# Kernel tuning notes

Measured on AMD Instinct MI355X. Metric: run time of the kernel, lower is better.

## Reference

```python
import jax, jax.numpy as jnp
import numpy as np

B, D, H = 131072, 8, 128


def setup_inputs() -> dict:
    key = jax.random.key(0)
    ks = jax.random.split(key, 8)
    s1 = 1.0 / np.sqrt(D + 1)
    s2 = 1.0 / np.sqrt(H)
    return {
        "z": jax.random.normal(ks[0], (B, D), dtype=jnp.float32),
        "logp_z": jnp.zeros((B, 1), dtype=jnp.float32),
        "t": jax.random.uniform(ks[1], (1,), dtype=jnp.float32),
        "W1": jax.random.normal(ks[2], (D + 1, H), dtype=jnp.float32) * s1,
        "b1": jnp.zeros((H,), dtype=jnp.float32),
        "W2": jax.random.normal(ks[3], (H, H), dtype=jnp.float32) * s2,
        "b2": jnp.zeros((H,), dtype=jnp.float32),
        "W3": jax.random.normal(ks[4], (H, D), dtype=jnp.float32) * s2,
        "b3": jnp.zeros((D,), dtype=jnp.float32),
    }


def _net_single(z_i, t_scalar, W1, b1, W2, b2, W3, b3):
    # z_i: [D] -> dz/dt: [D]; FFJORD-style MLP on concat([z, t])
    x = jnp.concatenate([z_i, t_scalar[None]])  # [D+1]
    h = jnp.tanh(x @ W1 + b1)
    h = jnp.tanh(h @ W2 + b2)
    return h @ W3 + b3


def reference(z, logp_z, t, W1, b1, W2, b2, W3, b3):
    t_scalar = t.reshape(())

    def f_i(z_i):
        return _net_single(z_i, t_scalar, W1, b1, W2, b2, W3, b3)

    # dz/dt for every sample (batched forward)
    dz_dt = jax.vmap(f_i)(z)  # [B, D]
    # Exact Jacobian trace: fused forward-mode batched Jacobian (replaces the
    # original's D sequential autograd.grad reverse-mode calls)
    jac = jax.vmap(jax.jacfwd(f_i))(z)  # [B, D, D]
    trace = jnp.einsum("bii->b", jac)  # [B]
    dlogp_z_dt = -trace[:, None]  # [B, 1]
    return (dz_dt, dlogp_z_dt)
```

## Files before the change

kernel.cpp:

```cpp
#include <hip/hip_runtime.h>
#include <hip/hip_bf16.h>

#define BATCH 131072
#define PITCH 136

typedef __bf16 bf16x8 __attribute__((ext_vector_type(8)));
typedef float floatx4 __attribute__((ext_vector_type(4)));

__device__ __forceinline__ float fast_tanh(float x) {
    float e = __expf(2.0f * x);
    return 1.0f - 2.0f * __builtin_amdgcn_rcpf(e + 1.0f);
}


__global__ void prep_kernel(const float* __restrict__ W1,
                            const float* __restrict__ W2,
                            const float* __restrict__ W3,
                            __bf16* __restrict__ ws) {
    int idx = blockIdx.x * 256 + threadIdx.x;
    if (idx < 16384) {
        int j = idx & 7, q = (idx >> 3) & 3, n = (idx >> 5) & 127, kb = idx >> 12;
        int k = kb * 32 + q * 8 + j;
        ws[idx] = (__bf16)W2[k * 128 + n];
        float c = 0.0f;
        #pragma unroll
        for (int d = 0; d < 8; ++d) c += W3[k * 8 + d] * W1[d * 128 + n];
        ws[16384 + idx] = (__bf16)(W2[n * 128 + k] * c);
    } else if (idx < 20480) {
        int t = idx - 16384;
        int j = t & 7, q = (t >> 3) & 3, n = t >> 5;
        int k = q * 8 + j;
        ws[32768 + t] = (k < 9) ? (__bf16)W1[k * 128 + n] : (__bf16)0.0f;
    } else if (idx < 22528) {
        int t = idx - 20480;
        int j = t & 7, q = (t >> 3) & 3, n = (t >> 5) & 15, kb = t >> 9;
        int k = kb * 32 + q * 8 + j;
        ws[36864 + t] = (n < 8) ? (__bf16)W3[k * 8 + n] : (__bf16)0.0f;
    }
}

__global__ __launch_bounds__(256, 2) void cnf_main(
        const float* __restrict__ z, const float* __restrict__ t_ptr,
        const float* __restrict__ b1g, const float* __restrict__ b2g,
        const float* __restrict__ b3g, const __bf16* __restrict__ ws,
        float* __restrict__ out) {
    __shared__ __bf16 sW2s[16384];
    __shared__ __bf16 sW1s[4096];
    __shared__ float sb1[128];
    __shared__ float sb2[128];
    __shared__ __bf16 tile[4][16 * PITCH];

    const int tid = threadIdx.x;
    {
        uint4* dst = (uint4*)sW2s;
        const uint4* src = (const uint4*)ws;
        for (int i = tid; i < 2048; i += 256) dst[i] = src[i];
        uint4* dst1 = (uint4*)sW1s;
        const uint4* src1 = (const uint4*)(ws + 32768);
        for (int i = tid; i < 512; i += 256) dst1[i] = src1[i];
        if (tid < 128) { sb1[tid] = b1g[tid]; sb2[tid] = b2g[tid]; }
    }
    __syncthreads();

    const int lane = tid & 63;
    const int w = tid >> 6;
    const int p = lane & 15;
    const int q = lane >> 4;
    __bf16* T = tile[w];
    const float tval = t_ptr[0];
    const float b3v = (p < 8) ? b3g[p] : 0.0f;
    const bf16x8* W2sv = (const bf16x8*)sW2s;
    const bf16x8* W1sv = (const bf16x8*)sW1s;
    const bf16x8* GTv  = (const bf16x8*)(ws + 16384);
    const bf16x8* W3v  = (const bf16x8*)(ws + 36864);

    for (int it = 0; it < 4; ++it) {
        const int s0 = blockIdx.x * 256 + it * 64 + w * 16;

        bf16x8 ax;
        #pragma unroll
        for (int j = 0; j < 8; ++j) ax[j] = (__bf16)0.0f;
        if (q == 0) {
            const float4 z0 = ((const float4*)(z + (size_t)(s0 + p) * 8))[0];
            const float4 z1 = ((const float4*)(z + (size_t)(s0 + p) * 8))[1];
            ax[0] = (__bf16)z0.x; ax[1] = (__bf16)z0.y;
            ax[2] = (__bf16)z0.z; ax[3] = (__bf16)z0.w;
            ax[4] = (__bf16)z1.x; ax[5] = (__bf16)z1.y;
            ax[6] = (__bf16)z1.z; ax[7] = (__bf16)z1.w;
        } else if (q == 1) {
            ax[0] = (__bf16)tval;
        }

        float a1c[32];
        #pragma unroll
        for (int nt = 0; nt < 8; ++nt) {
            const int n = nt * 16 + p;
            floatx4 acc = {0.f, 0.f, 0.f, 0.f};
            acc = __builtin_amdgcn_mfma_f32_16x16x32_bf16(ax, W1sv[n * 4 + q], acc, 0, 0, 0);
            const float bn = sb1[n];
            #pragma unroll
            for (int r = 0; r < 4; ++r) {
                const float h1 = fast_tanh(acc[r] + bn);
                a1c[nt * 4 + r] = __builtin_fmaf(-h1, h1, 1.0f);
                T[(q * 4 + r) * PITCH + n] = (__bf16)h1;
            }
        }
        bf16x8 ah[4];
        #pragma unroll
        for (int kb = 0; kb < 4; ++kb)
            ah[kb] = *(const bf16x8*)&T[p * PITCH + kb * 32 + q * 8];

        float h2c[32];
        #pragma unroll
        for (int nt = 0; nt < 8; ++nt) {
            const int n = nt * 16 + p;
            floatx4 acc = {0.f, 0.f, 0.f, 0.f};
            #pragma unroll
            for (int kb = 0; kb < 4; ++kb)
                acc = __builtin_amdgcn_mfma_f32_16x16x32_bf16(
                        ah[kb], W2sv[(kb * 128 + n) * 4 + q], acc, 0, 0, 0);
            const float bn = sb2[n];
            #pragma unroll
            for (int r = 0; r < 4; ++r) {
                const float h2 = fast_tanh(acc[r] + bn);
                h2c[nt * 4 + r] = h2;
                const float a2 = __builtin_fmaf(-h2, h2, 1.0f);
                T[(q * 4 + r) * PITCH + n] = (__bf16)a2;
            }
        }
        bf16x8 aa[4];
        #pragma unroll
        for (int kb = 0; kb < 4; ++kb)
            aa[kb] = *(const bf16x8*)&T[p * PITCH + kb * 32 + q * 8];

        float tr[4] = {0.f, 0.f, 0.f, 0.f};
        #pragma unroll
        for (int nt = 0; nt < 8; ++nt) {
            const int n = nt * 16 + p;
            floatx4 acc = {0.f, 0.f, 0.f, 0.f};
            #pragma unroll
            for (int kb = 0; kb < 4; ++kb)
                acc = __builtin_amdgcn_mfma_f32_16x16x32_bf16(
                        aa[kb], GTv[(kb * 128 + n) * 4 + q], acc, 0, 0, 0);
            #pragma unroll
            for (int r = 0; r < 4; ++r)
                tr[r] = __builtin_fmaf(a1c[nt * 4 + r], acc[r], tr[r]);
        }

        #pragma unroll
        for (int i = 0; i < 32; ++i)
            T[(q * 4 + (i & 3)) * PITCH + (i >> 2) * 16 + p] = (__bf16)h2c[i];
        bf16x8 ah2[4];
        #pragma unroll
        for (int kb = 0; kb < 4; ++kb)
            ah2[kb] = *(const bf16x8*)&T[p * PITCH + kb * 32 + q * 8];

        floatx4 acc3 = {0.f, 0.f, 0.f, 0.f};
        #pragma unroll
        for (int kb = 0; kb < 4; ++kb)
            acc3 = __builtin_amdgcn_mfma_f32_16x16x32_bf16(
                    ah2[kb], W3v[(kb * 16 + p) * 4 + q], acc3, 0, 0, 0);
        if (p < 8) {
            #pragma unroll
            for (int r = 0; r < 4; ++r)
                out[(size_t)(s0 + q * 4 + r) * 8 + p] = acc3[r] + b3v;
        }

        #pragma unroll
        for (int r = 0; r < 4; ++r) {
            float v = tr[r];
            v += __shfl_xor(v, 1, 64);
            v += __shfl_xor(v, 2, 64);
            v += __shfl_xor(v, 4, 64);
            v += __shfl_xor(v, 8, 64);
            tr[r] = v;
        }
        if (p == 0) {
            #pragma unroll
            for (int r = 0; r < 4; ++r)
                out[(size_t)BATCH * 8 + s0 + q * 4 + r] = -tr[r];
        }
    }
}

extern "C" void kernel_launch(void* const* d_in, const int* in_sizes, int n_in,
                              void* d_out, int out_size, void* d_ws, size_t ws_size,
                              hipStream_t stream) {
    const float* z  = (const float*)d_in[0];
    const float* t  = (const float*)d_in[2];
    const float* W1 = (const float*)d_in[3];
    const float* b1 = (const float*)d_in[4];
    const float* W2 = (const float*)d_in[5];
    const float* b2 = (const float*)d_in[6];
    const float* W3 = (const float*)d_in[7];
    const float* b3 = (const float*)d_in[8];
    __bf16* ws = (__bf16*)d_ws;
    float* out = (float*)d_out;

    prep_kernel<<<88, 256, 0, stream>>>(W1, W2, W3, ws);
    cnf_main<<<512, 256, 0, stream>>>(z, t, b1, b2, b3, ws, out);
}
```

Measured before the change: 104.0 us.

## Shrink LDS tile, pack activations, stage W3 in LDS, raise occupancy

The per-wave transpose tile shrinks from a 128-wide pitch to a 32-wide chunk that is reused for each k-block, and W3 is moved into shared memory. Biases now live in registers and the layer-1 derivative is kept as packed bf16 pairs, which cuts register use. The layer-2 tanh is now interleaved with the W3 MFMA, and the derivative is computed from the reloaded bf16 values. Together these aim for 3 blocks per CU and twice as many blocks (2 iterations each), at the cost of extra rounding of a1 and a2 to bf16.

```diff
diff --git a/kernel.cpp b/kernel.cpp
--- a/kernel.cpp
+++ b/kernel.cpp
@@ -2,7 +2,7 @@
 #include <hip/hip_bf16.h>
 
 #define BATCH 131072
-#define PITCH 136
+#define TP 40
 
 typedef __bf16 bf16x8 __attribute__((ext_vector_type(8)));
 typedef float floatx4 __attribute__((ext_vector_type(4)));
@@ -10,6 +10,18 @@
 __device__ __forceinline__ float fast_tanh(float x) {
     float e = __expf(2.0f * x);
     return 1.0f - 2.0f * __builtin_amdgcn_rcpf(e + 1.0f);
+}
+
+__device__ __forceinline__ unsigned int pk_bf16(float lo, float hi) {
+    unsigned short a = __builtin_bit_cast(unsigned short, (__bf16)lo);
+    unsigned short b = __builtin_bit_cast(unsigned short, (__bf16)hi);
+    return (unsigned int)a | ((unsigned int)b << 16);
+}
+__device__ __forceinline__ float unpk_lo(unsigned int u) {
+    return __builtin_bit_cast(float, u << 16);
+}
+__device__ __forceinline__ float unpk_hi(unsigned int u) {
+    return __builtin_bit_cast(float, u & 0xffff0000u);
 }
 
 
@@ -39,26 +51,25 @@
     }
 }
 
-__global__ __launch_bounds__(256, 2) void cnf_main(
+__global__ __launch_bounds__(256, 3) void cnf_main(
         const float* __restrict__ z, const float* __restrict__ t_ptr,
         const float* __restrict__ b1g, const float* __restrict__ b2g,
         const float* __restrict__ b3g, const __bf16* __restrict__ ws,
         float* __restrict__ out) {
     __shared__ __bf16 sW2s[16384];
     __shared__ __bf16 sW1s[4096];
-    __shared__ float sb1[128];
-    __shared__ float sb2[128];
-    __shared__ __bf16 tile[4][16 * PITCH];
+    __shared__ __bf16 sW3s[2048];
+    __shared__ __bf16 tile[4][16 * TP];
 
     const int tid = threadIdx.x;
     {
-        uint4* dst = (uint4*)sW2s;
-        const uint4* src = (const uint4*)ws;
-        for (int i = tid; i < 2048; i += 256) dst[i] = src[i];
-        uint4* dst1 = (uint4*)sW1s;
-        const uint4* src1 = (const uint4*)(ws + 32768);
-        for (int i = tid; i < 512; i += 256) dst1[i] = src1[i];
-        if (tid < 128) { sb1[tid] = b1g[tid]; sb2[tid] = b2g[tid]; }
+        const uint4* srcv = (const uint4*)ws;
+        uint4* dW2 = (uint4*)sW2s;
+        for (int i = tid; i < 2048; i += 256) dW2[i] = srcv[i];
+        uint4* dW1 = (uint4*)sW1s;
+        for (int i = tid; i < 512; i += 256) dW1[i] = srcv[4096 + i];
+        uint4* dW3 = (uint4*)sW3s;
+        dW3[tid] = srcv[4608 + tid];
     }
     __syncthreads();
 
@@ -71,18 +82,26 @@
     const float b3v = (p < 8) ? b3g[p] : 0.0f;
     const bf16x8* W2sv = (const bf16x8*)sW2s;
     const bf16x8* W1sv = (const bf16x8*)sW1s;
+    const bf16x8* W3sv = (const bf16x8*)sW3s;
     const bf16x8* GTv  = (const bf16x8*)(ws + 16384);
-    const bf16x8* W3v  = (const bf16x8*)(ws + 36864);
-
-    for (int it = 0; it < 4; ++it) {
-        const int s0 = blockIdx.x * 256 + it * 64 + w * 16;
-
+
+    float b1r[8], b2r[8];
+    #pragma unroll
+    for (int nt = 0; nt < 8; ++nt) {
+        b1r[nt] = b1g[nt * 16 + p];
+        b2r[nt] = b2g[nt * 16 + p];
+    }
+
+    bf16x8 axs[2];
+    #pragma unroll
+    for (int it = 0; it < 2; ++it) {
         bf16x8 ax;
         #pragma unroll
         for (int j = 0; j < 8; ++j) ax[j] = (__bf16)0.0f;
         if (q == 0) {
-            const float4 z0 = ((const float4*)(z + (size_t)(s0 + p) * 8))[0];
-            const float4 z1 = ((const float4*)(z + (size_t)(s0 + p) * 8))[1];
+            const int s = blockIdx.x * 128 + it * 64 + w * 16 + p;
+            const float4 z0 = ((const float4*)(z + (size_t)s * 8))[0];
+            const float4 z1 = ((const float4*)(z + (size_t)s * 8))[1];
             ax[0] = (__bf16)z0.x; ax[1] = (__bf16)z0.y;
             ax[2] = (__bf16)z0.z; ax[3] = (__bf16)z0.w;
             ax[4] = (__bf16)z1.x; ax[5] = (__bf16)z1.y;
@@ -90,76 +109,87 @@
         } else if (q == 1) {
             ax[0] = (__bf16)tval;
         }
-
-        float a1c[32];
+        axs[it] = ax;
+    }
+
+    for (int it = 0; it < 2; ++it) {
+        const int s0 = blockIdx.x * 128 + it * 64 + w * 16;
+
+        bf16x8 ah[4];
+        unsigned int a1p[16];
+        #pragma unroll
+        for (int kb = 0; kb < 4; ++kb) {
+            #pragma unroll
+            for (int h = 0; h < 2; ++h) {
+                const int nt = 2 * kb + h;
+                const int n = nt * 16 + p;
+                floatx4 acc = {0.f, 0.f, 0.f, 0.f};
+                acc = __builtin_amdgcn_mfma_f32_16x16x32_bf16(axs[it], W1sv[n * 4 + q], acc, 0, 0, 0);
+                float a1v[4];
+                #pragma unroll
+                for (int r = 0; r < 4; ++r) {
+                    const float h1 = fast_tanh(acc[r] + b1r[nt]);
+                    a1v[r] = __builtin_fmaf(-h1, h1, 1.0f);
+                    T[(q * 4 + r) * TP + h * 16 + p] = (__bf16)h1;
+                }
+                a1p[nt * 2]     = pk_bf16(a1v[0], a1v[1]);
+                a1p[nt * 2 + 1] = pk_bf16(a1v[2], a1v[3]);
+            }
+            ah[kb] = *(const bf16x8*)&T[p * TP + q * 8];
+        }
+
+        floatx4 acc[8];
+        #pragma unroll
+        for (int nt = 0; nt < 8; ++nt) acc[nt] = (floatx4){0.f, 0.f, 0.f, 0.f};
+        #pragma unroll
+        for (int kb = 0; kb < 4; ++kb) {
+            #pragma unroll
+            for (int nt = 0; nt < 8; ++nt)
+                acc[nt] = __builtin_amdgcn_mfma_f32_16x16x32_bf16(
+                        ah[kb], W2sv[(kb * 128 + nt * 16 + p) * 4 + q], acc[nt], 0, 0, 0);
+        }
+
+        bf16x8 av[4];
+        floatx4 acc3 = {0.f, 0.f, 0.f, 0.f};
+        #pragma unroll
+        for (int kb = 0; kb < 4; ++kb) {
+            #pragma unroll
+            for (int h = 0; h < 2; ++h) {
+                const int nt = 2 * kb + h;
+                #pragma unroll
+                for (int r = 0; r < 4; ++r) {
+                    const float h2 = fast_tanh(acc[nt][r] + b2r[nt]);
+                    T[(q * 4 + r) * TP + h * 16 + p] = (__bf16)h2;
+                }
+            }
+            av[kb] = *(const bf16x8*)&T[p * TP + q * 8];
+            acc3 = __builtin_amdgcn_mfma_f32_16x16x32_bf16(
+                    av[kb], W3sv[(kb * 16 + p) * 4 + q], acc3, 0, 0, 0);
+            #pragma unroll
+            for (int j = 0; j < 8; ++j) {
+                const float h2f = (float)av[kb][j];
+                av[kb][j] = (__bf16)__builtin_fmaf(-h2f, h2f, 1.0f);
+            }
+        }
+
+        #pragma unroll
+        for (int nt = 0; nt < 8; ++nt) acc[nt] = (floatx4){0.f, 0.f, 0.f, 0.f};
+        #pragma unroll
+        for (int kb = 0; kb < 4; ++kb) {
+            #pragma unroll
+            for (int nt = 0; nt < 8; ++nt)
+                acc[nt] = __builtin_amdgcn_mfma_f32_16x16x32_bf16(
+                        av[kb], GTv[(kb * 128 + nt * 16 + p) * 4 + q], acc[nt], 0, 0, 0);
+        }
+        float tr[4] = {0.f, 0.f, 0.f, 0.f};
         #pragma unroll
         for (int nt = 0; nt < 8; ++nt) {
-            const int n = nt * 16 + p;
-            floatx4 acc = {0.f, 0.f, 0.f, 0.f};
-            acc = __builtin_amdgcn_mfma_f32_16x16x32_bf16(ax, W1sv[n * 4 + q], acc, 0, 0, 0);
-            const float bn = sb1[n];
-            #pragma unroll
-            for (int r = 0; r < 4; ++r) {
-                const float h1 = fast_tanh(acc[r] + bn);
-                a1c[nt * 4 + r] = __builtin_fmaf(-h1, h1, 1.0f);
-                T[(q * 4 + r) * PITCH + n] = (__bf16)h1;
-            }
-        }
-        bf16x8 ah[4];
-        #pragma unroll
-        for (int kb = 0; kb < 4; ++kb)
-            ah[kb] = *(const bf16x8*)&T[p * PITCH + kb * 32 + q * 8];
-
-        float h2c[32];
-        #pragma unroll
-        for (int nt = 0; nt < 8; ++nt) {
-            const int n = nt * 16 + p;
-            floatx4 acc = {0.f, 0.f, 0.f, 0.f};
-            #pragma unroll
-            for (int kb = 0; kb < 4; ++kb)
-                acc = __builtin_amdgcn_mfma_f32_16x16x32_bf16(
-                        ah[kb], W2sv[(kb * 128 + n) * 4 + q], acc, 0, 0, 0);
-            const float bn = sb2[n];
-            #pragma unroll
-            for (int r = 0; r < 4; ++r) {
-                const float h2 = fast_tanh(acc[r] + bn);
-                h2c[nt * 4 + r] = h2;
-                const float a2 = __builtin_fmaf(-h2, h2, 1.0f);
-                T[(q * 4 + r) * PITCH + n] = (__bf16)a2;
-            }
-        }
-        bf16x8 aa[4];
-        #pragma unroll
-        for (int kb = 0; kb < 4; ++kb)
-            aa[kb] = *(const bf16x8*)&T[p * PITCH + kb * 32 + q * 8];
-
-        float tr[4] = {0.f, 0.f, 0.f, 0.f};
-        #pragma unroll
-        for (int nt = 0; nt < 8; ++nt) {
-            const int n = nt * 16 + p;
-            floatx4 acc = {0.f, 0.f, 0.f, 0.f};
-            #pragma unroll
-            for (int kb = 0; kb < 4; ++kb)
-                acc = __builtin_amdgcn_mfma_f32_16x16x32_bf16(
-                        aa[kb], GTv[(kb * 128 + n) * 4 + q], acc, 0, 0, 0);
-            #pragma unroll
-            for (int r = 0; r < 4; ++r)
-                tr[r] = __builtin_fmaf(a1c[nt * 4 + r], acc[r], tr[r]);
-        }
-
-        #pragma unroll
-        for (int i = 0; i < 32; ++i)
-            T[(q * 4 + (i & 3)) * PITCH + (i >> 2) * 16 + p] = (__bf16)h2c[i];
-        bf16x8 ah2[4];
-        #pragma unroll
-        for (int kb = 0; kb < 4; ++kb)
-            ah2[kb] = *(const bf16x8*)&T[p * PITCH + kb * 32 + q * 8];
-
-        floatx4 acc3 = {0.f, 0.f, 0.f, 0.f};
-        #pragma unroll
-        for (int kb = 0; kb < 4; ++kb)
-            acc3 = __builtin_amdgcn_mfma_f32_16x16x32_bf16(
-                    ah2[kb], W3v[(kb * 16 + p) * 4 + q], acc3, 0, 0, 0);
+            tr[0] = __builtin_fmaf(unpk_lo(a1p[nt * 2]),     acc[nt][0], tr[0]);
+            tr[1] = __builtin_fmaf(unpk_hi(a1p[nt * 2]),     acc[nt][1], tr[1]);
+            tr[2] = __builtin_fmaf(unpk_lo(a1p[nt * 2 + 1]), acc[nt][2], tr[2]);
+            tr[3] = __builtin_fmaf(unpk_hi(a1p[nt * 2 + 1]), acc[nt][3], tr[3]);
+        }
+
         if (p < 8) {
             #pragma unroll
             for (int r = 0; r < 4; ++r)
@@ -198,5 +228,5 @@
     float* out = (float*)d_out;
 
     prep_kernel<<<88, 256, 0, stream>>>(W1, W2, W3, ws);
-    cnf_main<<<512, 256, 0, stream>>>(z, t, b1, b2, b3, ws, out);
-}
+    cnf_main<<<1024, 256, 0, stream>>>(z, t, b1, b2, b3, ws, out);
+}
```

After: 104.6 us. No clear change (+0.5%).
